# Performance work log

Hardware: AMD Instinct MI355X
Metric: run time of the kernel (lower is better)

The kernel has to match this reference:

```python
import jax, jax.numpy as jnp
import numpy as np

B, NQ, D, H, L, P, FFN = 32, 300, 256, 8, 3, 4, 1024
SPATIAL = [(80, 80), (40, 40), (20, 20)]  # static multi-scale feature shapes (640px, strides 8/16/32)
S = sum(h * w for h, w in SPATIAL)  # 8400
HD = D // H


def _ln(x, g, b, eps=1e-5):
    m = jnp.mean(x, -1, keepdims=True)
    v = jnp.mean((x - m) ** 2, -1, keepdims=True)
    return (x - m) * jax.lax.rsqrt(v + eps) * g + b


def _grid_sample(img, grid):
    # img: (N,C,Hh,Ww); grid: (N,Q,Pp,2) in [-1,1]; bilinear, zeros padding, align_corners=False
    N, C, Hh, Ww = img.shape
    x = (grid[..., 0] + 1.0) * (Ww * 0.5) - 0.5
    y = (grid[..., 1] + 1.0) * (Hh * 0.5) - 0.5
    x0 = jnp.floor(x)
    y0 = jnp.floor(y)
    wx1 = x - x0
    wy1 = y - y0
    x0i = x0.astype(jnp.int32)
    y0i = y0.astype(jnp.int32)
    flat = img.reshape(N, C, Hh * Ww)
    Q, Pp = grid.shape[1], grid.shape[2]

    def corner(xi, yi, w):
        valid = (xi >= 0) & (xi < Ww) & (yi >= 0) & (yi < Hh)
        idx = jnp.clip(yi, 0, Hh - 1) * Ww + jnp.clip(xi, 0, Ww - 1)
        v = jnp.take_along_axis(flat, idx.reshape(N, 1, Q * Pp), axis=2).reshape(N, C, Q, Pp)
        return v * (w * valid)[:, None]

    return (corner(x0i, y0i, (1 - wx1) * (1 - wy1))
            + corner(x0i + 1, y0i, wx1 * (1 - wy1))
            + corner(x0i, y0i + 1, (1 - wx1) * wy1)
            + corner(x0i + 1, y0i + 1, wx1 * wy1))


def setup_inputs() -> dict:
    key = jax.random.key(0)
    ks = iter(jax.random.split(key, 32))
    inp = {
        'hidden_states': jax.random.normal(next(ks), (B, NQ, D), jnp.float32),
        'position_embeddings': jax.random.normal(next(ks), (B, NQ, D), jnp.float32),
        'reference_points': jax.random.uniform(next(ks), (B, NQ, 1, 4), jnp.float32, 0.1, 0.9),
        'encoder_hidden_states': jax.random.normal(next(ks), (B, S, D), jnp.float32),
    }
    for name, shape in [('Wq', (D, D)), ('Wk', (D, D)), ('Wv', (D, D)), ('Wo', (D, D)),
                        ('Woff', (D, H * L * P * 2)), ('Waw', (D, H * L * P)),
                        ('Wval', (D, D)), ('Wout', (D, D)), ('W1', (D, FFN)), ('W2', (FFN, D))]:
        inp[name] = jax.random.normal(next(ks), shape, jnp.float32) * 0.02
    for name, dim in [('bq', D), ('bk', D), ('bv', D), ('bo', D), ('boff', H * L * P * 2),
                      ('baw', H * L * P), ('bval', D), ('bout', D), ('b1', FFN), ('b2', D)]:
        inp[name] = jnp.zeros((dim,), jnp.float32)
    for g, bname in [('ln1_g', 'ln1_b'), ('ln2_g', 'ln2_b'), ('ln3_g', 'ln3_b')]:
        inp[g] = jnp.ones((D,), jnp.float32)
        inp[bname] = jnp.zeros((D,), jnp.float32)
    return inp


def reference(hidden_states, position_embeddings, reference_points, encoder_hidden_states,
              Wq, bq, Wk, bk, Wv, bv, Wo, bo, ln1_g, ln1_b,
              Woff, boff, Waw, baw, Wval, bval, Wout, bout, ln2_g, ln2_b,
              W1, b1, W2, b2, ln3_g, ln3_b):
    hs = hidden_states
    # ---- self attention (pos-embedded q/k, raw v) ----
    hp = hs + position_embeddings
    q = ((hp @ Wq + bq) * (HD ** -0.5)).reshape(B, NQ, H, HD)
    k = (hp @ Wk + bk).reshape(B, NQ, H, HD)
    v = (hs @ Wv + bv).reshape(B, NQ, H, HD)
    attn = jax.nn.softmax(jnp.einsum('bqhd,bkhd->bhqk', q, k), axis=-1)
    sa = jnp.einsum('bhqk,bkhd->bqhd', attn, v).reshape(B, NQ, D) @ Wo + bo
    hs = _ln(hs + sa, ln1_g, ln1_b)
    # ---- multi-scale deformable cross attention ----
    hp = hs + position_embeddings
    value = (encoder_hidden_states @ Wval + bval).reshape(B, S, H, HD)
    off = (hp @ Woff + boff).reshape(B, NQ, H, L, P, 2)
    aw = jax.nn.softmax((hp @ Waw + baw).reshape(B, NQ, H, L * P), axis=-1).reshape(B, NQ, H, L, P)
    ref = reference_points  # (B,NQ,1,4) boxes -> 4-coord branch
    loc = ref[:, :, None, :, None, :2] + off / P * ref[:, :, None, :, None, 2:] * 0.5
    grids = (2.0 * loc - 1.0).transpose(0, 2, 1, 3, 4, 5).reshape(B * H, NQ, L, P, 2)
    start = 0
    samples = []
    for lvl, (hh, ww) in enumerate(SPATIAL):
        v_l = value[:, start:start + hh * ww]  # (B,hw,H,HD)
        start += hh * ww
        v_l = v_l.transpose(0, 2, 3, 1).reshape(B * H, HD, hh, ww)
        samples.append(_grid_sample(v_l, grids[:, :, lvl]))  # (B*H,HD,NQ,P)
    sampled = jnp.stack(samples, axis=3).reshape(B * H, HD, NQ, L * P)
    w = aw.transpose(0, 2, 1, 3, 4).reshape(B * H, 1, NQ, L * P)
    ca = (sampled * w).sum(-1).reshape(B, H * HD, NQ).transpose(0, 2, 1) @ Wout + bout
    hs = _ln(hs + ca, ln2_g, ln2_b)
    # ---- FFN ----
    ff = jax.nn.relu(hs @ W1 + b1) @ W2 + b2
    return _ln(hs + ff, ln3_g, ln3_b)
```

## Files before the change

### kernel.cpp

```cpp
#include <hip/hip_runtime.h>
#include <hip/hip_bf16.h>

typedef unsigned int  uint32;
typedef unsigned short ushort16;
typedef __bf16 bfx8 __attribute__((ext_vector_type(8)));
typedef float  f32x4 __attribute__((ext_vector_type(4)));

typedef __attribute__((address_space(1))) const unsigned int gas_u32;
typedef __attribute__((address_space(3))) unsigned int las_u32;

#define B_   32
#define NQ_  300
#define D_   256
#define H_   8
#define HD_  32
#define L_   3
#define P_   4
#define S_   8400
#define FFN_ 1024
#define M1   (B_*NQ_)
#define MV   (B_*S_)
#define NQP  320
#define NQT  19

__device__ inline ushort16 f2bf(float x) {
  uint32 u = __float_as_uint(x);
  uint32 r = u + 0x7fffu + ((u >> 16) & 1u);
  return (ushort16)(r >> 16);
}
__device__ inline uint32 cvtpk(float lo, float hi) {
  uint32 r; asm("v_cvt_pk_bf16_f32 %0, %1, %2" : "=v"(r) : "v"(lo), "v"(hi)); return r;
}

__global__ __launch_bounds__(256) void rt_add(const float* __restrict__ a,
                                              const float* __restrict__ b,
                                              float* __restrict__ o, int n4)
{
  int i = blockIdx.x * 256 + threadIdx.x;
  if (i < n4) {
    float4 x = ((const float4*)a)[i];
    float4 y = ((const float4*)b)[i];
    float4 z; z.x = x.x + y.x; z.y = x.y + y.y; z.z = x.z + y.z; z.w = x.w + y.w;
    ((float4*)o)[i] = z;
  }
}

struct WPrep {
  const float* src[9];
  ushort16*    dst[9];
  int K[9], N[9], Npad[9], tileEnd[9];
  float scale[9];
  const float* wval; ushort16* wvalc;
  const float* bqs;  const float* bks;  float* bqk;
  const float* boffs; const float* baws; float* boffaw;
};

__global__ __launch_bounds__(256) void rt_wprep(WPrep a)
{
  __shared__ float t[32][33];
  int blk = blockIdx.x;
  if (blk < 904) {
    int wi = 0;
    while (blk >= a.tileEnd[wi]) wi++;
    int base = wi ? a.tileEnd[wi - 1] : 0;
    int idx = blk - base;
    int K = a.K[wi], N = a.N[wi];
    int ntx = a.Npad[wi] / 32;
    int n0 = (idx % ntx) * 32, k0 = (idx / ntx) * 32;
    float sc = a.scale[wi];
    const float* W = a.src[wi];
    ushort16* WT = a.dst[wi];
    int c = threadIdx.x & 31, r = threadIdx.x >> 5;
#pragma unroll
    for (int i = 0; i < 4; i++) {
      int nn = n0 + c;
      t[r + i * 8][c] = (nn < N) ? W[(size_t)(k0 + r + i * 8) * N + nn] : 0.f;
    }
    __syncthreads();
#pragma unroll
    for (int i = 0; i < 4; i++)
      WT[(size_t)(n0 + r + i * 8) * K + k0 + c] = f2bf(t[c][r + i * 8] * sc);
  } else if (blk < 936) {
    int gid = (blk - 904) * 256 + threadIdx.x;
    int c = gid >> 8, n = gid & 255;
    const float* W = a.wval;
    uint4 u;
    u.x = (uint32)f2bf(W[(c*8+0)*256 + n]) | ((uint32)f2bf(W[(c*8+1)*256 + n]) << 16);
    u.y = (uint32)f2bf(W[(c*8+2)*256 + n]) | ((uint32)f2bf(W[(c*8+3)*256 + n]) << 16);
    u.z = (uint32)f2bf(W[(c*8+4)*256 + n]) | ((uint32)f2bf(W[(c*8+5)*256 + n]) << 16);
    u.w = (uint32)f2bf(W[(c*8+6)*256 + n]) | ((uint32)f2bf(W[(c*8+7)*256 + n]) << 16);
    *(uint4*)&a.wvalc[(size_t)c * 2048 + n * 8] = u;
  } else if (blk == 936) {
    a.bqk[threadIdx.x] = a.bqs[threadIdx.x] * a.scale[0];
  } else if (blk == 937) {
    a.bqk[256 + threadIdx.x] = a.bks[threadIdx.x];
  } else if (blk == 938) {
    if (threadIdx.x < 192) a.boffaw[threadIdx.x] = a.boffs[threadIdx.x];
  } else {
    if (threadIdx.x < 96) a.boffaw[192 + threadIdx.x] = a.baws[threadIdx.x];
  }
}

__global__ __launch_bounds__(1024, 1) void rt_vgemm(
    const float* __restrict__ A, const ushort16* __restrict__ BC,
    const float* __restrict__ bias, ushort16* __restrict__ Vout)
{
  __shared__ __align__(16) char ldsB[131072];
  const int tid = threadIdx.x;
  const int lane = tid & 63, w = tid >> 6;
  const int l15 = lane & 15, l4 = lane >> 4;

#pragma unroll
  for (int i = 0; i < 8; ++i)
    __builtin_amdgcn_global_load_lds(
        (gas_u32*)(const void*)((const char*)BC + tid * 16 + i * 16384),
        (las_u32*)(void*)(&ldsB[tid * 16 + i * 16384]), 16, 0, 0);
  __syncthreads();

  const int wrow = w * 16 + l15;
  for (int t = blockIdx.x; t < MV / 256; t += 256) {
    const float* Ap = A + ((size_t)t * 256 + wrow) * 256 + l4 * 8;
    f32x4 aA = *(const f32x4*)(Ap);
    f32x4 aB = *(const f32x4*)(Ap + 4);
    f32x4 aC = *(const f32x4*)(Ap + 32);
    f32x4 aD = *(const f32x4*)(Ap + 36);
    f32x4 acc[16];
#pragma unroll
    for (int i = 0; i < 16; ++i) acc[i] = (f32x4){0.f, 0.f, 0.f, 0.f};

#pragma unroll
    for (int tt = 0; tt < 4; ++tt) {
      {
        uint4 u;
        u.x = cvtpk(aA[0], aA[1]); u.y = cvtpk(aA[2], aA[3]);
        u.z = cvtpk(aB[0], aB[1]); u.w = cvtpk(aB[2], aB[3]);
        bfx8 af = __builtin_bit_cast(bfx8, u);
        if (tt < 3) {
          aA = *(const f32x4*)(Ap + (2 * tt + 2) * 32);
          aB = *(const f32x4*)(Ap + (2 * tt + 2) * 32 + 4);
        }
        const char* bp = &ldsB[(2 * tt * 4 + l4) * 4096 + l15 * 16];
#pragma unroll
        for (int ni = 0; ni < 16; ++ni) {
          bfx8 bg = *(const bfx8*)(const void*)(bp + ni * 256);
          acc[ni] = __builtin_amdgcn_mfma_f32_16x16x32_bf16(bg, af, acc[ni], 0, 0, 0);
        }
      }
      {
        uint4 u;
        u.x = cvtpk(aC[0], aC[1]); u.y = cvtpk(aC[2], aC[3]);
        u.z = cvtpk(aD[0], aD[1]); u.w = cvtpk(aD[2], aD[3]);
        bfx8 af = __builtin_bit_cast(bfx8, u);
        if (tt < 3) {
          aC = *(const f32x4*)(Ap + (2 * tt + 3) * 32);
          aD = *(const f32x4*)(Ap + (2 * tt + 3) * 32 + 4);
        }
        const char* bp = &ldsB[((2 * tt + 1) * 4 + l4) * 4096 + l15 * 16];
#pragma unroll
        for (int ni = 0; ni < 16; ++ni) {
          bfx8 bg = *(const bfx8*)(const void*)(bp + ni * 256);
          acc[ni] = __builtin_amdgcn_mfma_f32_16x16x32_bf16(bg, af, acc[ni], 0, 0, 0);
        }
      }
    }
    int row = t * 256 + wrow;
    int bb = row / S_, s = row - bb * S_;
    ushort16* vb = Vout + (((size_t)bb * H_) * S_ + s) * HD_;
#pragma unroll
    for (int ni = 0; ni < 16; ++ni) {
      int col = ni * 16 + l4 * 4;
      f32x4 bv = *(const f32x4*)(bias + col);
      int hh = col >> 5, hd = col & 31;
      uint2 st;
      st.x = cvtpk(acc[ni][0] + bv[0], acc[ni][1] + bv[1]);
      st.y = cvtpk(acc[ni][2] + bv[2], acc[ni][3] + bv[3]);
      *(uint2*)(vb + (size_t)hh * S_ * HD_ + hd) = st;
    }
  }
}

#define GBM 128
#define GBN 128
#define GBK 32
#define LDP 40

__global__ __launch_bounds__(256) void rt_mgemm(
    const float* __restrict__ A, const ushort16* __restrict__ BT,
    const float* __restrict__ bias, float* __restrict__ C,
    ushort16* __restrict__ Sc, ushort16* __restrict__ Sc2,
    int M, int N, int K, float scale, int mode)
{
  __shared__ __align__(16) ushort16 As[GBM][LDP];
  __shared__ __align__(16) ushort16 Bs[GBN][LDP];
  const int tid  = threadIdx.x;
  const int lane = tid & 63;
  const int w    = tid >> 6;
  const int wr   = (w >> 1) * 64;
  const int wc   = (w & 1) * 64;
  const int bm   = blockIdx.y * GBM;
  const int bn   = blockIdx.x * GBN;
  const int l15  = lane & 15;
  const int l4   = lane >> 4;

  f32x4 acc[4][4];
#pragma unroll
  for (int i = 0; i < 4; i++)
#pragma unroll
    for (int j = 0; j < 4; j++)
      acc[i][j] = (f32x4){0.f, 0.f, 0.f, 0.f};

  const int arow = tid >> 3, akc = tid & 7;
  const int brow = tid >> 2, bkc = tid & 3;

  for (int k0 = 0; k0 < K; k0 += GBK) {
#pragma unroll
    for (int i = 0; i < 4; i++) {
      int row = arow + i * 32;
      f32x4 v = *(const f32x4*)(A + (size_t)(bm + row) * K + k0 + akc * 4);
      uint2 u;
      u.x = cvtpk(v.x, v.y);
      u.y = cvtpk(v.z, v.w);
      *(uint2*)(&As[row][akc * 4]) = u;
    }
#pragma unroll
    for (int i = 0; i < 2; i++) {
      int row = brow + i * 64;
      uint4 v = *(const uint4*)(BT + (size_t)(bn + row) * K + k0 + bkc * 8);
      *(uint4*)(&Bs[row][bkc * 8]) = v;
    }
    __syncthreads();

    bfx8 af[4], bg[4];
#pragma unroll
    for (int mi = 0; mi < 4; mi++)
      af[mi] = *(const bfx8*)(&As[wr + mi * 16 + l15][l4 * 8]);
#pragma unroll
    for (int ni = 0; ni < 4; ni++)
      bg[ni] = *(const bfx8*)(&Bs[wc + ni * 16 + l15][l4 * 8]);
#pragma unroll
    for (int mi = 0; mi < 4; mi++)
#pragma unroll
      for (int ni = 0; ni < 4; ni++)
        acc[mi][ni] = __builtin_amdgcn_mfma_f32_16x16x32_bf16(af[mi], bg[ni], acc[mi][ni], 0, 0, 0);
    __syncthreads();
  }

#pragma unroll
  for (int mi = 0; mi < 4; mi++) {
#pragma unroll
    for (int ni = 0; ni < 4; ni++) {
      int col = bn + wc + ni * 16 + l15;
      if (col >= N) continue;
      float bv = bias[col];
#pragma unroll
      for (int r = 0; r < 4; r++) {
        int row = bm + wr + mi * 16 + l4 * 4 + r;
        float vv = (acc[mi][ni][r] + bv) * scale;
        if (mode == 1) vv = fmaxf(vv, 0.f);
        if (mode == 3) {
          int bb = row / NQ_, q = row - bb * NQ_;
          int hh = col >> 5, hd = col & 31;
          Sc[(((size_t)bb * H_ + hh) * NQP + q) * HD_ + hd] = f2bf(vv);
        } else if (mode == 4) {
          int bb = row / NQ_, q = row - bb * NQ_;
          int hh = col >> 5, hd = col & 31;
          ushort16* d = (hh < 8) ? Sc : Sc2;
          d[(((size_t)bb * H_ + (hh & 7)) * NQP + q) * HD_ + hd] = f2bf(vv);
        } else {
          C[(size_t)row * N + col] = vv;
        }
      }
    }
  }
}

__global__ __launch_bounds__(256) void rt_vtr(const ushort16* __restrict__ vh,
                                              ushort16* __restrict__ vt)
{
  __shared__ ushort16 t[64][33];
  int bh = blockIdx.x;
  const ushort16* src = vh + (size_t)bh * NQP * HD_;
  ushort16* dst = vt + (size_t)bh * HD_ * NQP;
  int tid = threadIdx.x;
  int lrow = tid >> 2, lc8 = (tid & 3) * 8;
  int ohd = tid >> 3, oq8 = (tid & 7) * 8;
  for (int r0 = 0; r0 < NQP; r0 += 64) {
    uint4 v = *(const uint4*)(src + (size_t)(r0 + lrow) * HD_ + lc8);
    ushort16* tp = &t[lrow][lc8];
    tp[0] = (ushort16)(v.x & 0xffff); tp[1] = (ushort16)(v.x >> 16);
    tp[2] = (ushort16)(v.y & 0xffff); tp[3] = (ushort16)(v.y >> 16);
    tp[4] = (ushort16)(v.z & 0xffff); tp[5] = (ushort16)(v.z >> 16);
    tp[6] = (ushort16)(v.w & 0xffff); tp[7] = (ushort16)(v.w >> 16);
    __syncthreads();
    uint4 o;
    o.x = (uint32)t[oq8 + 0][ohd] | ((uint32)t[oq8 + 1][ohd] << 16);
    o.y = (uint32)t[oq8 + 2][ohd] | ((uint32)t[oq8 + 3][ohd] << 16);
    o.z = (uint32)t[oq8 + 4][ohd] | ((uint32)t[oq8 + 5][ohd] << 16);
    o.w = (uint32)t[oq8 + 6][ohd] | ((uint32)t[oq8 + 7][ohd] << 16);
    *(uint4*)(dst + (size_t)ohd * NQP + r0 + oq8) = o;
    __syncthreads();
  }
}

__global__ __launch_bounds__(256) void rt_fattn(
    const ushort16* __restrict__ qh, const ushort16* __restrict__ kh,
    const ushort16* __restrict__ vt, float* __restrict__ O)
{
  int gw  = blockIdx.x * 4 + (threadIdx.x >> 6);
  int bh  = gw / NQT, qt = gw - bh * NQT;
  int b   = bh >> 3, h = bh & 7;
  int lane = threadIdx.x & 63;
  int l15 = lane & 15, l4 = lane >> 4;
  int kb4 = l4 * 4;
  const ushort16* Qb = qh + (size_t)bh * NQP * HD_;
  const ushort16* Kb = kh + (size_t)bh * NQP * HD_;
  const ushort16* Vb = vt + (size_t)bh * HD_ * NQP;
  int q = qt * 16 + l15;

  bfx8 bgQ = *(const bfx8*)(const void*)(Qb + (size_t)q * HD_ + l4 * 8);
  f32x4 o0 = {0.f,0.f,0.f,0.f}, o1 = {0.f,0.f,0.f,0.f};
  float m = -1e30f, ssum = 0.f;

  for (int k0 = 0; k0 < NQP; k0 += 32) {
    bfx8 afk0 = *(const bfx8*)(const void*)(Kb + (size_t)(k0 + l15) * HD_ + l4 * 8);
    bfx8 afk1 = *(const bfx8*)(const void*)(Kb + (size_t)(k0 + 16 + l15) * HD_ + l4 * 8);
    f32x4 z = {0.f,0.f,0.f,0.f};
    f32x4 s0 = __builtin_amdgcn_mfma_f32_16x16x32_bf16(afk0, bgQ, z, 0, 0, 0);
    f32x4 s1 = __builtin_amdgcn_mfma_f32_16x16x32_bf16(afk1, bgQ, z, 0, 0, 0);
    int ka = k0 + kb4, kbb = k0 + 16 + kb4;
#pragma unroll
    for (int r = 0; r < 4; r++) {
      if (ka  + r >= NQ_) s0[r] = -1e30f;
      if (kbb + r >= NQ_) s1[r] = -1e30f;
    }
    float cm = fmaxf(fmaxf(fmaxf(s0[0], s0[1]), fmaxf(s0[2], s0[3])),
                     fmaxf(fmaxf(s1[0], s1[1]), fmaxf(s1[2], s1[3])));
    cm = fmaxf(cm, __shfl_xor(cm, 16));
    cm = fmaxf(cm, __shfl_xor(cm, 32));
    float nm = fmaxf(m, cm);
    float sc = __expf(m - nm);
    m = nm;
    f32x4 p0, p1;
#pragma unroll
    for (int r = 0; r < 4; r++) { p0[r] = __expf(s0[r] - m); p1[r] = __expf(s1[r] - m); }
    float ls = (p0[0]+p0[1]+p0[2]+p0[3]) + (p1[0]+p1[1]+p1[2]+p1[3]);
    ls += __shfl_xor(ls, 16);
    ls += __shfl_xor(ls, 32);
    ssum = ssum * sc + ls;

    uint32 t0w0 = cvtpk(p0[0], p0[1]);
    uint32 t0w1 = cvtpk(p0[2], p0[3]);
    uint32 t1w0 = cvtpk(p1[0], p1[1]);
    uint32 t1w1 = cvtpk(p1[2], p1[3]);
    int srcA = l15 + 32 * (l4 & 1);
    int srcB = srcA + 16;
    uint32 a00 = __shfl((int)t0w0, srcA), a01 = __shfl((int)t0w1, srcA);
    uint32 b00 = __shfl((int)t0w0, srcB), b01 = __shfl((int)t0w1, srcB);
    uint32 a10 = __shfl((int)t1w0, srcA), a11 = __shfl((int)t1w1, srcA);
    uint32 b10 = __shfl((int)t1w0, srcB), b11 = __shfl((int)t1w1, srcB);
    bool hi = (l4 >= 2);
    uint4 pw;
    pw.x = hi ? a10 : a00;
    pw.y = hi ? a11 : a01;
    pw.z = hi ? b10 : b00;
    pw.w = hi ? b11 : b01;
    bfx8 bgP = __builtin_bit_cast(bfx8, pw);

    bfx8 afv0 = *(const bfx8*)(const void*)(Vb + (size_t)l15 * NQP + k0 + l4 * 8);
    bfx8 afv1 = *(const bfx8*)(const void*)(Vb + (size_t)(16 + l15) * NQP + k0 + l4 * 8);
#pragma unroll
    for (int r = 0; r < 4; r++) { o0[r] *= sc; o1[r] *= sc; }
    o0 = __builtin_amdgcn_mfma_f32_16x16x32_bf16(afv0, bgP, o0, 0, 0, 0);
    o1 = __builtin_amdgcn_mfma_f32_16x16x32_bf16(afv1, bgP, o1, 0, 0, 0);
  }

  if (q < NQ_) {
    float inv = 1.f / ssum;
    float* op = O + ((size_t)(b * NQ_ + q)) * D_ + h * HD_ + kb4;
    f32x4 r0, r1;
#pragma unroll
    for (int r = 0; r < 4; r++) { r0[r] = o0[r] * inv; r1[r] = o1[r] * inv; }
    *(f32x4*)op = r0;
    *(f32x4*)(op + 16) = r1;
  }
}

__global__ __launch_bounds__(256) void rt_ln(
    const float* __restrict__ X, const float* __restrict__ R,
    const float* __restrict__ g, const float* __restrict__ be,
    float* __restrict__ O, int rows)
{
  int row = blockIdx.x * 4 + (threadIdx.x >> 6);
  int lane = threadIdx.x & 63;
  if (row >= rows) return;
  size_t base = (size_t)row * D_ + lane * 4;
  float4 x = *(const float4*)(X + base);
  float4 r = *(const float4*)(R + base);
  float v0 = x.x + r.x, v1 = x.y + r.y, v2 = x.z + r.z, v3 = x.w + r.w;
  float s = v0 + v1 + v2 + v3;
  float sq = v0*v0 + v1*v1 + v2*v2 + v3*v3;
#pragma unroll
  for (int o = 32; o >= 1; o >>= 1) { s += __shfl_xor(s, o); sq += __shfl_xor(sq, o); }
  float mean = s * (1.f / D_);
  float var  = sq * (1.f / D_) - mean * mean;
  float inv  = 1.f / sqrtf(var + 1e-5f);
  int c = lane * 4;
  float4 gv = *(const float4*)(g + c);
  float4 bv = *(const float4*)(be + c);
  float4 o4;
  o4.x = (v0 - mean) * inv * gv.x + bv.x;
  o4.y = (v1 - mean) * inv * gv.y + bv.y;
  o4.z = (v2 - mean) * inv * gv.z + bv.z;
  o4.w = (v3 - mean) * inv * gv.w + bv.w;
  *(float4*)(O + base) = o4;
}

__device__ inline void rt_acc8(const ushort16* p, float wgt, float* acc) {
  uint4 v = *(const uint4*)(const void*)p;
  acc[0] += wgt * __uint_as_float(v.x << 16);
  acc[1] += wgt * __uint_as_float(v.x & 0xffff0000u);
  acc[2] += wgt * __uint_as_float(v.y << 16);
  acc[3] += wgt * __uint_as_float(v.y & 0xffff0000u);
  acc[4] += wgt * __uint_as_float(v.z << 16);
  acc[5] += wgt * __uint_as_float(v.z & 0xffff0000u);
  acc[6] += wgt * __uint_as_float(v.w << 16);
  acc[7] += wgt * __uint_as_float(v.w & 0xffff0000u);
}

__global__ __launch_bounds__(256) void rt_deform(
    const ushort16* __restrict__ value,
    const float* __restrict__ offaw,
    const float* __restrict__ ref,
    float* __restrict__ O)
{
  int gid = blockIdx.x * 256 + threadIdx.x;
  int hd0 = (gid & 3) * 8;
  int bqh = gid >> 2;
  int h   = bqh & 7;
  int bq  = bqh >> 3;
  int b   = bq / NQ_;
  const float* rp = ref + (size_t)bq * 4;
  float rx = rp[0], ry = rp[1];
  float rw = rp[2] * 0.125f, rh = rp[3] * 0.125f;
  const float* op = offaw + (size_t)bq * 288 + h * 24;
  const float* ap = offaw + (size_t)bq * 288 + 192 + h * 12;
  float e[12]; float mx = -1e30f;
#pragma unroll
  for (int i = 0; i < 12; i++) { e[i] = ap[i]; mx = fmaxf(mx, e[i]); }
  float ssum = 0.f;
#pragma unroll
  for (int i = 0; i < 12; i++) { e[i] = __expf(e[i] - mx); ssum += e[i]; }
  float sinv = 1.f / ssum;

  const ushort16* vb = value + ((size_t)b * H_ + h) * (size_t)S_ * HD_ + hd0;
  float acc[8];
#pragma unroll
  for (int i = 0; i < 8; i++) acc[i] = 0.f;
  const int starts[3] = {0, 6400, 8000};
  const int dims[3]   = {80, 40, 20};
#pragma unroll
  for (int l = 0; l < L_; l++) {
    const int Wl = dims[l];
    const ushort16* vl = vb + (size_t)starts[l] * HD_;
#pragma unroll
    for (int p = 0; p < P_; p++) {
      int ip = l * P_ + p;
      float wgt = e[ip] * sinv;
      float x = (rx + op[ip*2+0] * rw) * Wl - 0.5f;
      float y = (ry + op[ip*2+1] * rh) * Wl - 0.5f;
      float x0f = floorf(x), y0f = floorf(y);
      int   x0 = (int)x0f,  y0 = (int)y0f;
      float wx1 = x - x0f, wy1 = y - y0f;
      float wx0 = 1.f - wx1, wy0 = 1.f - wy1;
      bool xok0 = (x0 >= 0) & (x0 < Wl), xok1 = (x0+1 >= 0) & (x0+1 < Wl);
      bool yok0 = (y0 >= 0) & (y0 < Wl), yok1 = (y0+1 >= 0) & (y0+1 < Wl);
      const ushort16* r0p = vl + (size_t)(y0 * Wl) * HD_;
      const ushort16* r1p = r0p + (size_t)Wl * HD_;
      if (xok0 & yok0) rt_acc8(r0p + (size_t)x0 * HD_,     wgt * wx0 * wy0, acc);
      if (xok1 & yok0) rt_acc8(r0p + (size_t)(x0+1) * HD_, wgt * wx1 * wy0, acc);
      if (xok0 & yok1) rt_acc8(r1p + (size_t)x0 * HD_,     wgt * wx0 * wy1, acc);
      if (xok1 & yok1) rt_acc8(r1p + (size_t)(x0+1) * HD_, wgt * wx1 * wy1, acc);
    }
  }
  float* outp = O + (size_t)bq * D_ + h * HD_ + hd0;
  float4 a0, a1;
  a0.x = acc[0]; a0.y = acc[1]; a0.z = acc[2]; a0.w = acc[3];
  a1.x = acc[4]; a1.y = acc[5]; a1.z = acc[6]; a1.w = acc[7];
  *(float4*)outp = a0;
  *(float4*)(outp + 4) = a1;
}

extern "C" void kernel_launch(void* const* d_in, const int* in_sizes, int n_in,
                              void* d_out, int out_size, void* d_ws, size_t ws_size,
                              hipStream_t stream)
{
  const float* hs   = (const float*)d_in[0];
  const float* pos  = (const float*)d_in[1];
  const float* ref  = (const float*)d_in[2];
  const float* ehs  = (const float*)d_in[3];
  const float* Wq   = (const float*)d_in[4];
  const float* Wk   = (const float*)d_in[5];
  const float* Wv   = (const float*)d_in[6];
  const float* Wo   = (const float*)d_in[7];
  const float* Woff = (const float*)d_in[8];
  const float* Waw  = (const float*)d_in[9];
  const float* Wval = (const float*)d_in[10];
  const float* Wout = (const float*)d_in[11];
  const float* W1   = (const float*)d_in[12];
  const float* W2   = (const float*)d_in[13];
  const float* bq   = (const float*)d_in[14];
  const float* bk   = (const float*)d_in[15];
  const float* bvv  = (const float*)d_in[16];
  const float* bo   = (const float*)d_in[17];
  const float* boff = (const float*)d_in[18];
  const float* baw  = (const float*)d_in[19];
  const float* bval = (const float*)d_in[20];
  const float* bout = (const float*)d_in[21];
  const float* b1   = (const float*)d_in[22];
  const float* b2   = (const float*)d_in[23];
  const float* ln1g = (const float*)d_in[24];
  const float* ln1b = (const float*)d_in[25];
  const float* ln2g = (const float*)d_in[26];
  const float* ln2b = (const float*)d_in[27];
  const float* ln3g = (const float*)d_in[28];
  const float* ln3b = (const float*)d_in[29];
  float* out = (float*)d_out;

  float* ws = (float*)d_ws;
  ushort16* value = (ushort16*)ws;
  float* hp     = ws + 34406400;
  float* t0     = ws + 36864000;
  float* t1     = ws + 39321600;
  float* hs1    = ws + 41779200;
  float* hs2    = ws + 44236800;
  float* offawb = ws + 46694400;
  float* ffn1   = ws + 49459200;
  ushort16* qh = (ushort16*)(ws + 59289600);
  ushort16* kh = (ushort16*)(ws + 60600320);
  ushort16* vh = (ushort16*)(ws + 61911040);
  ushort16* vt = (ushort16*)(ws + 63221760);
  ushort16* wbase  = (ushort16*)(ws + 64532480);
  ushort16* WqkT   = wbase;
  ushort16* WvT    = WqkT   + 131072;
  ushort16* WoT    = WvT    + 65536;
  ushort16* WoffawT= WoT    + 65536;
  ushort16* WoutT  = WoffawT+ 98304;
  ushort16* W1T    = WoutT  + 65536;
  ushort16* W2T    = W1T    + 262144;
  ushort16* WvalC  = W2T    + 262144;
  float* bqk    = (float*)(WvalC + 65536);
  float* boffaw = bqk + 512;

  const float qscale = 0.17677669529663687f;

  WPrep a;
  a.src[0]=Wq;   a.dst[0]=WqkT;            a.K[0]=256;  a.N[0]=256;  a.Npad[0]=256; a.scale[0]=qscale;
  a.src[1]=Wk;   a.dst[1]=WqkT+65536;      a.K[1]=256;  a.N[1]=256;  a.Npad[1]=256; a.scale[1]=1.f;
  a.src[2]=Wv;   a.dst[2]=WvT;             a.K[2]=256;  a.N[2]=256;  a.Npad[2]=256; a.scale[2]=1.f;
  a.src[3]=Wo;   a.dst[3]=WoT;             a.K[3]=256;  a.N[3]=256;  a.Npad[3]=256; a.scale[3]=1.f;
  a.src[4]=Woff; a.dst[4]=WoffawT;         a.K[4]=256;  a.N[4]=192;  a.Npad[4]=192; a.scale[4]=1.f;
  a.src[5]=Waw;  a.dst[5]=WoffawT+49152;   a.K[5]=256;  a.N[5]=96;   a.Npad[5]=96;  a.scale[5]=1.f;
  a.src[6]=Wout; a.dst[6]=WoutT;           a.K[6]=256;  a.N[6]=256;  a.Npad[6]=256; a.scale[6]=1.f;
  a.src[7]=W1;   a.dst[7]=W1T;             a.K[7]=256;  a.N[7]=1024; a.Npad[7]=1024;a.scale[7]=1.f;
  a.src[8]=W2;   a.dst[8]=W2T;             a.K[8]=1024; a.N[8]=256;  a.Npad[8]=256; a.scale[8]=1.f;
  int cum = 0;
  int tiles[9] = {64, 64, 64, 64, 48, 24, 64, 256, 256};
  for (int i = 0; i < 9; i++) { cum += tiles[i]; a.tileEnd[i] = cum; }
  a.wval = Wval; a.wvalc = WvalC;
  a.bqs = bq; a.bks = bk; a.bqk = bqk;
  a.boffs = boff; a.baws = baw; a.boffaw = boffaw;
  rt_wprep<<<dim3(940), 256, 0, stream>>>(a);

  rt_vgemm<<<dim3(256), 1024, 0, stream>>>(ehs, WvalC, bval, value);

  rt_add<<<dim3(M1*D_/4/256), 256, 0, stream>>>(hs, pos, hp, M1*D_/4);
  rt_mgemm<<<dim3(4, M1/GBM), 256, 0, stream>>>(hp, WqkT, bqk, nullptr, qh, kh, M1, 512, D_, 1.f, 4);
  rt_mgemm<<<dim3(2, M1/GBM), 256, 0, stream>>>(hs, WvT, bvv, nullptr, vh, vh, M1, D_, D_, 1.f, 3);
  rt_vtr<<<dim3(B_*H_), 256, 0, stream>>>(vh, vt);
  rt_fattn<<<dim3(B_*H_*NQT/4), 256, 0, stream>>>(qh, kh, vt, t0);
  rt_mgemm<<<dim3(2, M1/GBM), 256, 0, stream>>>(t0, WoT, bo, t1, nullptr, nullptr, M1, D_, D_, 1.f, 0);
  rt_ln<<<dim3(M1/4), 256, 0, stream>>>(hs, t1, ln1g, ln1b, hs1, M1);
  rt_add<<<dim3(M1*D_/4/256), 256, 0, stream>>>(hs1, pos, hp, M1*D_/4);
  rt_mgemm<<<dim3(3, M1/GBM), 256, 0, stream>>>(hp, WoffawT, boffaw, offawb, nullptr, nullptr, M1, 288, D_, 1.f, 0);
  rt_deform<<<dim3(M1*H_*4/256), 256, 0, stream>>>(value, offawb, ref, t0);
  rt_mgemm<<<dim3(2, M1/GBM), 256, 0, stream>>>(t0, WoutT, bout, t1, nullptr, nullptr, M1, D_, D_, 1.f, 0);
  rt_ln<<<dim3(M1/4), 256, 0, stream>>>(hs1, t1, ln2g, ln2b, hs2, M1);
  rt_mgemm<<<dim3(8, M1/GBM), 256, 0, stream>>>(hs2, W1T, b1, ffn1, nullptr, nullptr, M1, FFN_, D_, 1.f, 1);
  rt_mgemm<<<dim3(2, M1/GBM), 256, 0, stream>>>(ffn1, W2T, b2, t1, nullptr, nullptr, M1, D_, FFN_, 1.f, 0);
  rt_ln<<<dim3(M1/4), 256, 0, stream>>>(hs2, t1, ln3g, ln3b, out, M1);
}
```

Measured before the change: 387.5 us.

## Replace LDS-tiled GEMM with register-streaming MFMA GEMM and fuse positional add

Swaps the 128x128 LDS-tiled bf16 GEMM for a kernel that streams A rows straight from global memory into registers, with prefetch, and reads pre-packed k-chunked bf16 weight images directly. Each wave handles 16 rows across up to 256 columns. The hs+pos additions are folded into the GEMM A-load, which removes the two elementwise add kernels and the hp buffer. Weight prep now emits the k-chunk-of-8 layout for every matrix, and Q/K and off/aw weights are concatenated into single images. The risk is that the new kernel does no LDS reuse of B across waves, so weight traffic is served only from cache.

```diff
diff --git a/kernel.cpp b/kernel.cpp
--- a/kernel.cpp
+++ b/kernel.cpp
@@ -32,69 +32,41 @@
   uint32 r; asm("v_cvt_pk_bf16_f32 %0, %1, %2" : "=v"(r) : "v"(lo), "v"(hi)); return r;
 }
 
-__global__ __launch_bounds__(256) void rt_add(const float* __restrict__ a,
-                                              const float* __restrict__ b,
-                                              float* __restrict__ o, int n4)
-{
-  int i = blockIdx.x * 256 + threadIdx.x;
-  if (i < n4) {
-    float4 x = ((const float4*)a)[i];
-    float4 y = ((const float4*)b)[i];
-    float4 z; z.x = x.x + y.x; z.y = x.y + y.y; z.z = x.z + y.z; z.w = x.w + y.w;
-    ((float4*)o)[i] = z;
-  }
-}
-
 struct WPrep {
-  const float* src[9];
-  ushort16*    dst[9];
-  int K[9], N[9], Npad[9], tileEnd[9];
-  float scale[9];
-  const float* wval; ushort16* wvalc;
-  const float* bqs;  const float* bks;  float* bqk;
+  const float* srcA[8]; const float* srcB[8];
+  ushort16*    dst[8];
+  int K[8], Nimg[8], split[8], NsrcA[8], NsrcB[8], blkEnd[8];
+  float scaleA[8];
+  const float* bqs; const float* bks; float* bqk;
   const float* boffs; const float* baws; float* boffaw;
+  float qscale;
 };
 
 __global__ __launch_bounds__(256) void rt_wprep(WPrep a)
 {
-  __shared__ float t[32][33];
   int blk = blockIdx.x;
-  if (blk < 904) {
+  if (blk < 484) {
     int wi = 0;
-    while (blk >= a.tileEnd[wi]) wi++;
-    int base = wi ? a.tileEnd[wi - 1] : 0;
-    int idx = blk - base;
-    int K = a.K[wi], N = a.N[wi];
-    int ntx = a.Npad[wi] / 32;
-    int n0 = (idx % ntx) * 32, k0 = (idx / ntx) * 32;
-    float sc = a.scale[wi];
-    const float* W = a.src[wi];
-    ushort16* WT = a.dst[wi];
-    int c = threadIdx.x & 31, r = threadIdx.x >> 5;
-#pragma unroll
-    for (int i = 0; i < 4; i++) {
-      int nn = n0 + c;
-      t[r + i * 8][c] = (nn < N) ? W[(size_t)(k0 + r + i * 8) * N + nn] : 0.f;
-    }
-    __syncthreads();
-#pragma unroll
-    for (int i = 0; i < 4; i++)
-      WT[(size_t)(n0 + r + i * 8) * K + k0 + c] = f2bf(t[c][r + i * 8] * sc);
-  } else if (blk < 936) {
-    int gid = (blk - 904) * 256 + threadIdx.x;
-    int c = gid >> 8, n = gid & 255;
-    const float* W = a.wval;
+    while (blk >= a.blkEnd[wi]) wi++;
+    int base = wi ? a.blkEnd[wi - 1] : 0;
+    int g = (blk - base) * 256 + threadIdx.x;
+    int Nimg = a.Nimg[wi];
+    int kc = g / Nimg, n = g - kc * Nimg;
+    const float* src; int cs, Ns; float sc;
+    if (n < a.split[wi]) { src = a.srcA[wi]; cs = n; Ns = a.NsrcA[wi]; sc = a.scaleA[wi]; }
+    else                 { src = a.srcB[wi]; cs = n - a.split[wi]; Ns = a.NsrcB[wi]; sc = 1.f; }
+    const float* p = src + (size_t)(kc * 8) * Ns + cs;
     uint4 u;
-    u.x = (uint32)f2bf(W[(c*8+0)*256 + n]) | ((uint32)f2bf(W[(c*8+1)*256 + n]) << 16);
-    u.y = (uint32)f2bf(W[(c*8+2)*256 + n]) | ((uint32)f2bf(W[(c*8+3)*256 + n]) << 16);
-    u.z = (uint32)f2bf(W[(c*8+4)*256 + n]) | ((uint32)f2bf(W[(c*8+5)*256 + n]) << 16);
-    u.w = (uint32)f2bf(W[(c*8+6)*256 + n]) | ((uint32)f2bf(W[(c*8+7)*256 + n]) << 16);
-    *(uint4*)&a.wvalc[(size_t)c * 2048 + n * 8] = u;
-  } else if (blk == 936) {
-    a.bqk[threadIdx.x] = a.bqs[threadIdx.x] * a.scale[0];
-  } else if (blk == 937) {
+    u.x = (uint32)f2bf(p[0*Ns]*sc) | ((uint32)f2bf(p[1*Ns]*sc) << 16);
+    u.y = (uint32)f2bf(p[2*Ns]*sc) | ((uint32)f2bf(p[3*Ns]*sc) << 16);
+    u.z = (uint32)f2bf(p[4*Ns]*sc) | ((uint32)f2bf(p[5*Ns]*sc) << 16);
+    u.w = (uint32)f2bf(p[6*Ns]*sc) | ((uint32)f2bf(p[7*Ns]*sc) << 16);
+    *(uint4*)&a.dst[wi][(size_t)g * 8] = u;
+  } else if (blk == 484) {
+    a.bqk[threadIdx.x] = a.bqs[threadIdx.x] * a.qscale;
+  } else if (blk == 485) {
     a.bqk[256 + threadIdx.x] = a.bks[threadIdx.x];
-  } else if (blk == 938) {
+  } else if (blk == 486) {
     if (threadIdx.x < 192) a.boffaw[threadIdx.x] = a.boffs[threadIdx.x];
   } else {
     if (threadIdx.x < 96) a.boffaw[192 + threadIdx.x] = a.baws[threadIdx.x];
@@ -179,97 +151,84 @@
   }
 }
 
-#define GBM 128
-#define GBN 128
-#define GBK 32
-#define LDP 40
-
-__global__ __launch_bounds__(256) void rt_mgemm(
-    const float* __restrict__ A, const ushort16* __restrict__ BT,
-    const float* __restrict__ bias, float* __restrict__ C,
-    ushort16* __restrict__ Sc, ushort16* __restrict__ Sc2,
-    int M, int N, int K, float scale, int mode)
-{
-  __shared__ __align__(16) ushort16 As[GBM][LDP];
-  __shared__ __align__(16) ushort16 Bs[GBN][LDP];
-  const int tid  = threadIdx.x;
-  const int lane = tid & 63;
-  const int w    = tid >> 6;
-  const int wr   = (w >> 1) * 64;
-  const int wc   = (w & 1) * 64;
-  const int bm   = blockIdx.y * GBM;
-  const int bn   = blockIdx.x * GBN;
-  const int l15  = lane & 15;
-  const int l4   = lane >> 4;
-
-  f32x4 acc[4][4];
-#pragma unroll
-  for (int i = 0; i < 4; i++)
-#pragma unroll
-    for (int j = 0; j < 4; j++)
-      acc[i][j] = (f32x4){0.f, 0.f, 0.f, 0.f};
-
-  const int arow = tid >> 3, akc = tid & 7;
-  const int brow = tid >> 2, bkc = tid & 3;
-
-  for (int k0 = 0; k0 < K; k0 += GBK) {
-#pragma unroll
-    for (int i = 0; i < 4; i++) {
-      int row = arow + i * 32;
-      f32x4 v = *(const f32x4*)(A + (size_t)(bm + row) * K + k0 + akc * 4);
-      uint2 u;
-      u.x = cvtpk(v.x, v.y);
-      u.y = cvtpk(v.z, v.w);
-      *(uint2*)(&As[row][akc * 4]) = u;
-    }
-#pragma unroll
-    for (int i = 0; i < 2; i++) {
-      int row = brow + i * 64;
-      uint4 v = *(const uint4*)(BT + (size_t)(bn + row) * K + k0 + bkc * 8);
-      *(uint4*)(&Bs[row][bkc * 8]) = v;
-    }
-    __syncthreads();
-
-    bfx8 af[4], bg[4];
-#pragma unroll
-    for (int mi = 0; mi < 4; mi++)
-      af[mi] = *(const bfx8*)(&As[wr + mi * 16 + l15][l4 * 8]);
-#pragma unroll
-    for (int ni = 0; ni < 4; ni++)
-      bg[ni] = *(const bfx8*)(&Bs[wc + ni * 16 + l15][l4 * 8]);
-#pragma unroll
-    for (int mi = 0; mi < 4; mi++)
-#pragma unroll
-      for (int ni = 0; ni < 4; ni++)
-        acc[mi][ni] = __builtin_amdgcn_mfma_f32_16x16x32_bf16(af[mi], bg[ni], acc[mi][ni], 0, 0, 0);
-    __syncthreads();
-  }
-
-#pragma unroll
-  for (int mi = 0; mi < 4; mi++) {
-#pragma unroll
-    for (int ni = 0; ni < 4; ni++) {
-      int col = bn + wc + ni * 16 + l15;
-      if (col >= N) continue;
-      float bv = bias[col];
-#pragma unroll
-      for (int r = 0; r < 4; r++) {
-        int row = bm + wr + mi * 16 + l4 * 4 + r;
-        float vv = (acc[mi][ni][r] + bv) * scale;
-        if (mode == 1) vv = fmaxf(vv, 0.f);
-        if (mode == 3) {
-          int bb = row / NQ_, q = row - bb * NQ_;
-          int hh = col >> 5, hd = col & 31;
-          Sc[(((size_t)bb * H_ + hh) * NQP + q) * HD_ + hd] = f2bf(vv);
-        } else if (mode == 4) {
-          int bb = row / NQ_, q = row - bb * NQ_;
-          int hh = col >> 5, hd = col & 31;
-          ushort16* d = (hh < 8) ? Sc : Sc2;
-          d[(((size_t)bb * H_ + (hh & 7)) * NQP + q) * HD_ + hd] = f2bf(vv);
-        } else {
-          C[(size_t)row * N + col] = vv;
-        }
+__global__ __launch_bounds__(256) void rt_sgemm(
+    const float* __restrict__ A, const float* __restrict__ A2,
+    const ushort16* __restrict__ Wimg, const float* __restrict__ bias,
+    float* __restrict__ C, ushort16* __restrict__ Sc, ushort16* __restrict__ Sc2,
+    int Nimg, int K, int Nc, int mode)
+{
+  const int lane = threadIdx.x & 63, w = threadIdx.x >> 6;
+  const int l15 = lane & 15, l4 = lane >> 4;
+  const int n0 = blockIdx.x * 256;
+  const int NB = min(256, Nimg - n0);
+  const int row = blockIdx.y * 64 + w * 16 + l15;
+  const int nk = K / 32;
+
+  const float* Ap  = A + (size_t)row * K + l4 * 8;
+  const float* Ap2 = A2 ? A2 + (size_t)row * K + l4 * 8 : nullptr;
+
+  f32x4 acc[16];
+#pragma unroll
+  for (int i = 0; i < 16; ++i) acc[i] = (f32x4){0.f, 0.f, 0.f, 0.f};
+
+  f32x4 a0 = *(const f32x4*)(Ap);
+  f32x4 a1 = *(const f32x4*)(Ap + 4);
+  if (A2) {
+    f32x4 b0 = *(const f32x4*)(Ap2);
+    f32x4 b1 = *(const f32x4*)(Ap2 + 4);
+#pragma unroll
+    for (int r = 0; r < 4; r++) { a0[r] += b0[r]; a1[r] += b1[r]; }
+  }
+
+  for (int t = 0; t < nk; ++t) {
+    f32x4 p0 = {0.f,0.f,0.f,0.f}, p1 = {0.f,0.f,0.f,0.f};
+    if (t + 1 < nk) {
+      p0 = *(const f32x4*)(Ap + (t + 1) * 32);
+      p1 = *(const f32x4*)(Ap + (t + 1) * 32 + 4);
+      if (A2) {
+        f32x4 q0 = *(const f32x4*)(Ap2 + (t + 1) * 32);
+        f32x4 q1 = *(const f32x4*)(Ap2 + (t + 1) * 32 + 4);
+#pragma unroll
+        for (int r = 0; r < 4; r++) { p0[r] += q0[r]; p1[r] += q1[r]; }
       }
+    }
+    uint4 u;
+    u.x = cvtpk(a0[0], a0[1]); u.y = cvtpk(a0[2], a0[3]);
+    u.z = cvtpk(a1[0], a1[1]); u.w = cvtpk(a1[2], a1[3]);
+    bfx8 af = __builtin_bit_cast(bfx8, u);
+    const ushort16* bp = Wimg + ((size_t)(t * 4 + l4) * Nimg + n0 + l15) * 8;
+#pragma unroll
+    for (int ni = 0; ni < 16; ++ni) {
+      if (ni * 16 < NB) {
+        bfx8 bg = *(const bfx8*)(const void*)(bp + ni * 128);
+        acc[ni] = __builtin_amdgcn_mfma_f32_16x16x32_bf16(bg, af, acc[ni], 0, 0, 0);
+      }
+    }
+    a0 = p0; a1 = p1;
+  }
+
+  int bb = row / NQ_, q = row - bb * NQ_;
+#pragma unroll
+  for (int ni = 0; ni < 16; ++ni) {
+    if (ni * 16 >= NB) continue;
+    int col = n0 + ni * 16 + l4 * 4;
+    f32x4 bv = *(const f32x4*)(bias + col);
+    f32x4 vv;
+#pragma unroll
+    for (int r = 0; r < 4; r++) vv[r] = acc[ni][r] + bv[r];
+    if (mode == 1) {
+#pragma unroll
+      for (int r = 0; r < 4; r++) vv[r] = fmaxf(vv[r], 0.f);
+    }
+    if (mode <= 1) {
+      *(f32x4*)(C + (size_t)row * Nc + col) = vv;
+    } else {
+      int hh = col >> 5, hd = col & 31;
+      ushort16* d = (mode == 3) ? Sc : ((hh < 8) ? Sc : Sc2);
+      uint2 st;
+      st.x = cvtpk(vv[0], vv[1]);
+      st.y = cvtpk(vv[2], vv[3]);
+      *(uint2*)(d + (((size_t)bb * H_ + (hh & 7)) * NQP + q) * HD_ + hd) = st;
     }
   }
 }
@@ -528,64 +487,58 @@
 
   float* ws = (float*)d_ws;
   ushort16* value = (ushort16*)ws;
-  float* hp     = ws + 34406400;
-  float* t0     = ws + 36864000;
-  float* t1     = ws + 39321600;
-  float* hs1    = ws + 41779200;
-  float* hs2    = ws + 44236800;
-  float* offawb = ws + 46694400;
-  float* ffn1   = ws + 49459200;
-  ushort16* qh = (ushort16*)(ws + 59289600);
-  ushort16* kh = (ushort16*)(ws + 60600320);
-  ushort16* vh = (ushort16*)(ws + 61911040);
-  ushort16* vt = (ushort16*)(ws + 63221760);
-  ushort16* wbase  = (ushort16*)(ws + 64532480);
-  ushort16* WqkT   = wbase;
-  ushort16* WvT    = WqkT   + 131072;
-  ushort16* WoT    = WvT    + 65536;
-  ushort16* WoffawT= WoT    + 65536;
-  ushort16* WoutT  = WoffawT+ 98304;
-  ushort16* W1T    = WoutT  + 65536;
-  ushort16* W2T    = W1T    + 262144;
-  ushort16* WvalC  = W2T    + 262144;
-  float* bqk    = (float*)(WvalC + 65536);
-  float* boffaw = bqk + 512;
+  float* t0     = ws + 34406400;
+  float* t1     = ws + 36864000;
+  float* hs1    = ws + 39321600;
+  float* hs2    = ws + 41779200;
+  float* offawb = ws + 44236800;
+  float* ffn1   = ws + 47001600;
+  ushort16* qh = (ushort16*)(ws + 56832000);
+  ushort16* kh = (ushort16*)(ws + 58142720);
+  ushort16* vh = (ushort16*)(ws + 59453440);
+  ushort16* vt = (ushort16*)(ws + 60764160);
+  ushort16* WqkC   = (ushort16*)(ws + 62074880);
+  ushort16* WvC    = (ushort16*)(ws + 62140416);
+  ushort16* WoC    = (ushort16*)(ws + 62173184);
+  ushort16* WoffawC= (ushort16*)(ws + 62205952);
+  ushort16* WoutC  = (ushort16*)(ws + 62242816);
+  ushort16* W1C    = (ushort16*)(ws + 62275584);
+  ushort16* W2C    = (ushort16*)(ws + 62406656);
+  ushort16* WvalC  = (ushort16*)(ws + 62537728);
+  float* bqk    = ws + 62570496;
+  float* boffaw = ws + 62571008;
 
   const float qscale = 0.17677669529663687f;
 
   WPrep a;
-  a.src[0]=Wq;   a.dst[0]=WqkT;            a.K[0]=256;  a.N[0]=256;  a.Npad[0]=256; a.scale[0]=qscale;
-  a.src[1]=Wk;   a.dst[1]=WqkT+65536;      a.K[1]=256;  a.N[1]=256;  a.Npad[1]=256; a.scale[1]=1.f;
-  a.src[2]=Wv;   a.dst[2]=WvT;             a.K[2]=256;  a.N[2]=256;  a.Npad[2]=256; a.scale[2]=1.f;
-  a.src[3]=Wo;   a.dst[3]=WoT;             a.K[3]=256;  a.N[3]=256;  a.Npad[3]=256; a.scale[3]=1.f;
-  a.src[4]=Woff; a.dst[4]=WoffawT;         a.K[4]=256;  a.N[4]=192;  a.Npad[4]=192; a.scale[4]=1.f;
-  a.src[5]=Waw;  a.dst[5]=WoffawT+49152;   a.K[5]=256;  a.N[5]=96;   a.Npad[5]=96;  a.scale[5]=1.f;
-  a.src[6]=Wout; a.dst[6]=WoutT;           a.K[6]=256;  a.N[6]=256;  a.Npad[6]=256; a.scale[6]=1.f;
-  a.src[7]=W1;   a.dst[7]=W1T;             a.K[7]=256;  a.N[7]=1024; a.Npad[7]=1024;a.scale[7]=1.f;
-  a.src[8]=W2;   a.dst[8]=W2T;             a.K[8]=1024; a.N[8]=256;  a.Npad[8]=256; a.scale[8]=1.f;
+  a.srcA[0]=Wq;   a.srcB[0]=Wk;  a.dst[0]=WqkC;    a.K[0]=256;  a.Nimg[0]=512;  a.split[0]=256; a.NsrcA[0]=256;  a.NsrcB[0]=256; a.scaleA[0]=qscale;
+  a.srcA[1]=Wv;   a.srcB[1]=Wv;  a.dst[1]=WvC;     a.K[1]=256;  a.Nimg[1]=256;  a.split[1]=256; a.NsrcA[1]=256;  a.NsrcB[1]=256; a.scaleA[1]=1.f;
+  a.srcA[2]=Wo;   a.srcB[2]=Wo;  a.dst[2]=WoC;     a.K[2]=256;  a.Nimg[2]=256;  a.split[2]=256; a.NsrcA[2]=256;  a.NsrcB[2]=256; a.scaleA[2]=1.f;
+  a.srcA[3]=Woff; a.srcB[3]=Waw; a.dst[3]=WoffawC; a.K[3]=256;  a.Nimg[3]=288;  a.split[3]=192; a.NsrcA[3]=192;  a.NsrcB[3]=96;  a.scaleA[3]=1.f;
+  a.srcA[4]=Wout; a.srcB[4]=Wout;a.dst[4]=WoutC;   a.K[4]=256;  a.Nimg[4]=256;  a.split[4]=256; a.NsrcA[4]=256;  a.NsrcB[4]=256; a.scaleA[4]=1.f;
+  a.srcA[5]=W1;   a.srcB[5]=W1;  a.dst[5]=W1C;     a.K[5]=256;  a.Nimg[5]=1024; a.split[5]=1024;a.NsrcA[5]=1024; a.NsrcB[5]=1024;a.scaleA[5]=1.f;
+  a.srcA[6]=W2;   a.srcB[6]=W2;  a.dst[6]=W2C;     a.K[6]=1024; a.Nimg[6]=256;  a.split[6]=256; a.NsrcA[6]=256;  a.NsrcB[6]=256; a.scaleA[6]=1.f;
+  a.srcA[7]=Wval; a.srcB[7]=Wval;a.dst[7]=WvalC;   a.K[7]=256;  a.Nimg[7]=256;  a.split[7]=256; a.NsrcA[7]=256;  a.NsrcB[7]=256; a.scaleA[7]=1.f;
   int cum = 0;
-  int tiles[9] = {64, 64, 64, 64, 48, 24, 64, 256, 256};
-  for (int i = 0; i < 9; i++) { cum += tiles[i]; a.tileEnd[i] = cum; }
-  a.wval = Wval; a.wvalc = WvalC;
+  int blks[8] = {64, 32, 32, 36, 32, 128, 128, 32};
+  for (int i = 0; i < 8; i++) { cum += blks[i]; a.blkEnd[i] = cum; }
   a.bqs = bq; a.bks = bk; a.bqk = bqk;
-  a.boffs = boff; a.baws = baw; a.boffaw = boffaw;
-  rt_wprep<<<dim3(940), 256, 0, stream>>>(a);
+  a.boffs = boff; a.baws = baw; a.boffaw = boffaw; a.qscale = qscale;
+  rt_wprep<<<dim3(488), 256, 0, stream>>>(a);
 
   rt_vgemm<<<dim3(256), 1024, 0, stream>>>(ehs, WvalC, bval, value);
 
-  rt_add<<<dim3(M1*D_/4/256), 256, 0, stream>>>(hs, pos, hp, M1*D_/4);
-  rt_mgemm<<<dim3(4, M1/GBM), 256, 0, stream>>>(hp, WqkT, bqk, nullptr, qh, kh, M1, 512, D_, 1.f, 4);
-  rt_mgemm<<<dim3(2, M1/GBM), 256, 0, stream>>>(hs, WvT, bvv, nullptr, vh, vh, M1, D_, D_, 1.f, 3);
+  rt_sgemm<<<dim3(2, 150), 256, 0, stream>>>(hs, pos, WqkC, bqk, nullptr, qh, kh, 512, 256, 0, 4);
+  rt_sgemm<<<dim3(1, 150), 256, 0, stream>>>(hs, nullptr, WvC, bvv, nullptr, vh, nullptr, 256, 256, 0, 3);
   rt_vtr<<<dim3(B_*H_), 256, 0, stream>>>(vh, vt);
   rt_fattn<<<dim3(B_*H_*NQT/4), 256, 0, stream>>>(qh, kh, vt, t0);
-  rt_mgemm<<<dim3(2, M1/GBM), 256, 0, stream>>>(t0, WoT, bo, t1, nullptr, nullptr, M1, D_, D_, 1.f, 0);
+  rt_sgemm<<<dim3(1, 150), 256, 0, stream>>>(t0, nullptr, WoC, bo, t1, nullptr, nullptr, 256, 256, 256, 0);
   rt_ln<<<dim3(M1/4), 256, 0, stream>>>(hs, t1, ln1g, ln1b, hs1, M1);
-  rt_add<<<dim3(M1*D_/4/256), 256, 0, stream>>>(hs1, pos, hp, M1*D_/4);
-  rt_mgemm<<<dim3(3, M1/GBM), 256, 0, stream>>>(hp, WoffawT, boffaw, offawb, nullptr, nullptr, M1, 288, D_, 1.f, 0);
+  rt_sgemm<<<dim3(2, 150), 256, 0, stream>>>(hs1, pos, WoffawC, boffaw, offawb, nullptr, nullptr, 288, 256, 288, 0);
   rt_deform<<<dim3(M1*H_*4/256), 256, 0, stream>>>(value, offawb, ref, t0);
-  rt_mgemm<<<dim3(2, M1/GBM), 256, 0, stream>>>(t0, WoutT, bout, t1, nullptr, nullptr, M1, D_, D_, 1.f, 0);
+  rt_sgemm<<<dim3(1, 150), 256, 0, stream>>>(t0, nullptr, WoutC, bout, t1, nullptr, nullptr, 256, 256, 256, 0);
   rt_ln<<<dim3(M1/4), 256, 0, stream>>>(hs1, t1, ln2g, ln2b, hs2, M1);
-  rt_mgemm<<<dim3(8, M1/GBM), 256, 0, stream>>>(hs2, W1T, b1, ffn1, nullptr, nullptr, M1, FFN_, D_, 1.f, 1);
-  rt_mgemm<<<dim3(2, M1/GBM), 256, 0, stream>>>(ffn1, W2T, b2, t1, nullptr, nullptr, M1, D_, FFN_, 1.f, 0);
+  rt_sgemm<<<dim3(4, 150), 256, 0, stream>>>(hs2, nullptr, W1C, b1, ffn1, nullptr, nullptr, 1024, 256, 1024, 1);
+  rt_sgemm<<<dim3(1, 150), 256, 0, stream>>>(ffn1, nullptr, W2C, b2, t1, nullptr, nullptr, 256, 1024, 256, 0);
   rt_ln<<<dim3(M1/4), 256, 0, stream>>>(hs2, t1, ln3g, ln3b, out, M1);
 }
```

New measurement: 856.6 us. 2.21x slower.

## Fuse positional add into GEMM loads and split-K the narrow GEMMs

Applied to the files above, without the earlier changes.

Removes the two standalone elementwise add kernels by letting the GEMM add a second A operand while loading tiles. It also runs the N=256 GEMMs (Wo, Wout, W2) as a two-way split-K over grid z. Each split writes its own partial buffer, and the following LayerNorm sums both partials. The aim is fewer launches and less memory traffic, and more blocks for the narrow GEMMs that otherwise fill few CUs. In exchange, the partial buffers add extra writes and reads, and the hp+pos load now happens once per column tile.

```diff
diff --git a/kernel.cpp b/kernel.cpp
--- a/kernel.cpp
+++ b/kernel.cpp
@@ -30,19 +30,6 @@
 }
 __device__ inline uint32 cvtpk(float lo, float hi) {
   uint32 r; asm("v_cvt_pk_bf16_f32 %0, %1, %2" : "=v"(r) : "v"(lo), "v"(hi)); return r;
-}
-
-__global__ __launch_bounds__(256) void rt_add(const float* __restrict__ a,
-                                              const float* __restrict__ b,
-                                              float* __restrict__ o, int n4)
-{
-  int i = blockIdx.x * 256 + threadIdx.x;
-  if (i < n4) {
-    float4 x = ((const float4*)a)[i];
-    float4 y = ((const float4*)b)[i];
-    float4 z; z.x = x.x + y.x; z.y = x.y + y.y; z.z = x.z + y.z; z.w = x.w + y.w;
-    ((float4*)o)[i] = z;
-  }
 }
 
 struct WPrep {
@@ -185,10 +172,11 @@
 #define LDP 40
 
 __global__ __launch_bounds__(256) void rt_mgemm(
-    const float* __restrict__ A, const ushort16* __restrict__ BT,
-    const float* __restrict__ bias, float* __restrict__ C,
+    const float* __restrict__ A, const float* __restrict__ A2,
+    const ushort16* __restrict__ BT, const float* __restrict__ bias,
+    float* __restrict__ C, float* __restrict__ C2,
     ushort16* __restrict__ Sc, ushort16* __restrict__ Sc2,
-    int M, int N, int K, float scale, int mode)
+    int M, int N, int K, int klen, float scale, int mode)
 {
   __shared__ __align__(16) ushort16 As[GBM][LDP];
   __shared__ __align__(16) ushort16 Bs[GBN][LDP];
@@ -199,6 +187,8 @@
   const int wc   = (w & 1) * 64;
   const int bm   = blockIdx.y * GBM;
   const int bn   = blockIdx.x * GBN;
+  const int kz   = blockIdx.z;
+  const int kb   = kz * klen;
   const int l15  = lane & 15;
   const int l4   = lane >> 4;
 
@@ -212,11 +202,16 @@
   const int arow = tid >> 3, akc = tid & 7;
   const int brow = tid >> 2, bkc = tid & 3;
 
-  for (int k0 = 0; k0 < K; k0 += GBK) {
+  for (int k0 = kb; k0 < kb + klen; k0 += GBK) {
 #pragma unroll
     for (int i = 0; i < 4; i++) {
       int row = arow + i * 32;
       f32x4 v = *(const f32x4*)(A + (size_t)(bm + row) * K + k0 + akc * 4);
+      if (A2) {
+        f32x4 v2 = *(const f32x4*)(A2 + (size_t)(bm + row) * K + k0 + akc * 4);
+#pragma unroll
+        for (int r = 0; r < 4; r++) v[r] += v2[r];
+      }
       uint2 u;
       u.x = cvtpk(v.x, v.y);
       u.y = cvtpk(v.z, v.w);
@@ -245,13 +240,14 @@
     __syncthreads();
   }
 
+  float* Cp = kz ? C2 : C;
 #pragma unroll
   for (int mi = 0; mi < 4; mi++) {
 #pragma unroll
     for (int ni = 0; ni < 4; ni++) {
       int col = bn + wc + ni * 16 + l15;
       if (col >= N) continue;
-      float bv = bias[col];
+      float bv = kz ? 0.f : bias[col];
 #pragma unroll
       for (int r = 0; r < 4; r++) {
         int row = bm + wr + mi * 16 + l4 * 4 + r;
@@ -267,7 +263,7 @@
           ushort16* d = (hh < 8) ? Sc : Sc2;
           d[(((size_t)bb * H_ + (hh & 7)) * NQP + q) * HD_ + hd] = f2bf(vv);
         } else {
-          C[(size_t)row * N + col] = vv;
+          Cp[(size_t)row * N + col] = vv;
         }
       }
     }
@@ -385,8 +381,9 @@
   }
 }
 
-__global__ __launch_bounds__(256) void rt_ln(
-    const float* __restrict__ X, const float* __restrict__ R,
+__global__ __launch_bounds__(256) void rt_ln2(
+    const float* __restrict__ X, const float* __restrict__ R1,
+    const float* __restrict__ R2,
     const float* __restrict__ g, const float* __restrict__ be,
     float* __restrict__ O, int rows)
 {
@@ -395,8 +392,12 @@
   if (row >= rows) return;
   size_t base = (size_t)row * D_ + lane * 4;
   float4 x = *(const float4*)(X + base);
-  float4 r = *(const float4*)(R + base);
+  float4 r = *(const float4*)(R1 + base);
   float v0 = x.x + r.x, v1 = x.y + r.y, v2 = x.z + r.z, v3 = x.w + r.w;
+  if (R2) {
+    float4 r2 = *(const float4*)(R2 + base);
+    v0 += r2.x; v1 += r2.y; v2 += r2.z; v3 += r2.w;
+  }
   float s = v0 + v1 + v2 + v3;
   float sq = v0*v0 + v1*v1 + v2*v2 + v3*v3;
 #pragma unroll
@@ -528,7 +529,7 @@
 
   float* ws = (float*)d_ws;
   ushort16* value = (ushort16*)ws;
-  float* hp     = ws + 34406400;
+  float* t2     = ws + 34406400;
   float* t0     = ws + 36864000;
   float* t1     = ws + 39321600;
   float* hs1    = ws + 41779200;
@@ -573,19 +574,17 @@
 
   rt_vgemm<<<dim3(256), 1024, 0, stream>>>(ehs, WvalC, bval, value);
 
-  rt_add<<<dim3(M1*D_/4/256), 256, 0, stream>>>(hs, pos, hp, M1*D_/4);
-  rt_mgemm<<<dim3(4, M1/GBM), 256, 0, stream>>>(hp, WqkT, bqk, nullptr, qh, kh, M1, 512, D_, 1.f, 4);
-  rt_mgemm<<<dim3(2, M1/GBM), 256, 0, stream>>>(hs, WvT, bvv, nullptr, vh, vh, M1, D_, D_, 1.f, 3);
+  rt_mgemm<<<dim3(4, M1/GBM, 1), 256, 0, stream>>>(hs, pos, WqkT, bqk, nullptr, nullptr, qh, kh, M1, 512, 256, 256, 1.f, 4);
+  rt_mgemm<<<dim3(2, M1/GBM, 1), 256, 0, stream>>>(hs, nullptr, WvT, bvv, nullptr, nullptr, vh, nullptr, M1, 256, 256, 256, 1.f, 3);
   rt_vtr<<<dim3(B_*H_), 256, 0, stream>>>(vh, vt);
   rt_fattn<<<dim3(B_*H_*NQT/4), 256, 0, stream>>>(qh, kh, vt, t0);
-  rt_mgemm<<<dim3(2, M1/GBM), 256, 0, stream>>>(t0, WoT, bo, t1, nullptr, nullptr, M1, D_, D_, 1.f, 0);
-  rt_ln<<<dim3(M1/4), 256, 0, stream>>>(hs, t1, ln1g, ln1b, hs1, M1);
-  rt_add<<<dim3(M1*D_/4/256), 256, 0, stream>>>(hs1, pos, hp, M1*D_/4);
-  rt_mgemm<<<dim3(3, M1/GBM), 256, 0, stream>>>(hp, WoffawT, boffaw, offawb, nullptr, nullptr, M1, 288, D_, 1.f, 0);
+  rt_mgemm<<<dim3(2, M1/GBM, 2), 256, 0, stream>>>(t0, nullptr, WoT, bo, t1, t2, nullptr, nullptr, M1, 256, 256, 128, 1.f, 0);
+  rt_ln2<<<dim3(M1/4), 256, 0, stream>>>(hs, t1, t2, ln1g, ln1b, hs1, M1);
+  rt_mgemm<<<dim3(3, M1/GBM, 1), 256, 0, stream>>>(hs1, pos, WoffawT, boffaw, offawb, nullptr, nullptr, nullptr, M1, 288, 256, 256, 1.f, 0);
   rt_deform<<<dim3(M1*H_*4/256), 256, 0, stream>>>(value, offawb, ref, t0);
-  rt_mgemm<<<dim3(2, M1/GBM), 256, 0, stream>>>(t0, WoutT, bout, t1, nullptr, nullptr, M1, D_, D_, 1.f, 0);
-  rt_ln<<<dim3(M1/4), 256, 0, stream>>>(hs1, t1, ln2g, ln2b, hs2, M1);
-  rt_mgemm<<<dim3(8, M1/GBM), 256, 0, stream>>>(hs2, W1T, b1, ffn1, nullptr, nullptr, M1, FFN_, D_, 1.f, 1);
-  rt_mgemm<<<dim3(2, M1/GBM), 256, 0, stream>>>(ffn1, W2T, b2, t1, nullptr, nullptr, M1, D_, FFN_, 1.f, 0);
-  rt_ln<<<dim3(M1/4), 256, 0, stream>>>(hs2, t1, ln3g, ln3b, out, M1);
-}
+  rt_mgemm<<<dim3(2, M1/GBM, 2), 256, 0, stream>>>(t0, nullptr, WoutT, bout, t1, t2, nullptr, nullptr, M1, 256, 256, 128, 1.f, 0);
+  rt_ln2<<<dim3(M1/4), 256, 0, stream>>>(hs1, t1, t2, ln2g, ln2b, hs2, M1);
+  rt_mgemm<<<dim3(8, M1/GBM, 1), 256, 0, stream>>>(hs2, nullptr, W1T, b1, ffn1, nullptr, nullptr, nullptr, M1, FFN_, 256, 256, 1.f, 1);
+  rt_mgemm<<<dim3(2, M1/GBM, 2), 256, 0, stream>>>(ffn1, nullptr, W2T, b2, t1, t2, nullptr, nullptr, M1, 256, 1024, 512, 1.f, 0);
+  rt_ln2<<<dim3(M1/4), 256, 0, stream>>>(hs2, t1, t2, ln3g, ln3b, out, M1);
+}
```

Result: no change. 394.1 us (+1.7%).
